# Kernel tuning notes

Measured on AMD Instinct MI355X. Metric: run time of the kernel, lower is better.

Reference implementation:

```python
import jax, jax.numpy as jnp
import numpy as np
from jax import lax

B_SZ, L, D, N, R = 1, 4096, 768, 16, 48  # R = dt_rank = ceil(D/16)


def _soft_clamp(x, lo=1e-4, hi=10.0):
    center = (hi + lo) / 2.0
    half_range = (hi - lo) / 2.0
    return center + half_range * jnp.tanh((x - center) / half_range)


def setup_inputs() -> dict:
    key = jax.random.key(0)
    ks = jax.random.split(key, 6)
    x = jax.random.normal(ks[0], (B_SZ, L, D), jnp.float32)
    # A_log init: log(1..N) broadcast over D (HiPPO-style S4D-real init)
    A_log = jnp.log(jnp.broadcast_to(jnp.arange(1, N + 1, dtype=jnp.float32), (D, N)))
    D_param = jnp.ones((D,), jnp.float32)
    # lecun_normal kernels
    W_bc = jax.random.normal(ks[1], (D, 2 * N), jnp.float32) / np.sqrt(D).astype(np.float32)
    W_dt = jax.random.normal(ks[2], (D, R), jnp.float32) / np.sqrt(D).astype(np.float32)
    W_dtp = jax.random.normal(ks[3], (R, D), jnp.float32) / np.sqrt(R).astype(np.float32)
    # dt bias init: inverse-softplus of uniform(dt_min, dt_max)
    dt = jax.random.uniform(ks[4], (D,), jnp.float32, 0.001, 0.1)
    dt = jnp.clip(dt, 1e-4)
    b_dt = dt + jnp.log(-jnp.expm1(-dt))
    rms_scale = jnp.ones((D,), jnp.float32)  # RMSNorm learnable scale
    return {"x": x, "A_log": A_log, "D_param": D_param, "W_bc": W_bc,
            "W_dt": W_dt, "W_dtp": W_dtp, "b_dt": b_dt, "rms_scale": rms_scale}


def reference(x, A_log, D_param, W_bc, W_dt, W_dtp, b_dt, rms_scale):
    n = A_log.shape[1]
    A = -jnp.exp(A_log)                                   # (D, N)
    bc = x @ W_bc                                         # (B, L, 2N)
    B_sel, C_sel = bc[..., :n], bc[..., n:]               # (B, L, N) each
    # delta = softplus(dt_proj(x_dt)) -> RMSNorm -> soft_clamp  (tustin mode)
    delta = jax.nn.softplus((x @ W_dt) @ W_dtp + b_dt)    # (B, L, D)
    delta = delta * lax.rsqrt(jnp.mean(delta * delta, axis=-1, keepdims=True) + 1e-6) * rms_scale
    delta = _soft_clamp(delta, 1e-4, 10.0)
    # Bilinear (Tustin) discretization, all fp32 already
    dE = delta[..., None]                                 # (B, L, D, 1)
    half = 0.5 * dE * A                                   # (B, L, D, N)
    denom = 1.0 - half
    A_bar = (1.0 + half) / denom                          # (B, L, D, N)
    B_bar = jnp.sqrt(dE) * B_sel[:, :, None, :] / denom   # (B, L, D, N)
    # trapezoidal input averaging
    x_prev = jnp.concatenate([jnp.zeros_like(x[:, :1]), x[:, :-1]], axis=1)
    x_in = 0.5 * (x + x_prev)                             # (B, L, D)
    Bx = B_bar * x_in[..., None]                          # (B, L, D, N)

    def op(left, right):
        a_l, b_l = left
        a_r, b_r = right
        return (a_r * a_l, a_r * b_l + b_r)

    _, all_h = lax.associative_scan(op, (A_bar, Bx), axis=1)
    y = jnp.sum(C_sel[:, :, None, :] * all_h, axis=-1)    # (B, L, D)
    return y + D_param * x
```

## Files before the change

### kernel.cpp

```cpp
#include <hip/hip_runtime.h>
#include <math.h>

#define LSEQ 4096
#define DD 768
#define NST 16
#define RNK 48
#define TCH 64
#define NCH (LSEQ / TCH)
#define KSTEPS 24
#define NTILES 5
#define WFRAG_N (KSTEPS * NTILES * 64 * 8)
#define WDTP_N  (2 * RNK * 64 * 8)

typedef __attribute__((ext_vector_type(8))) short bf16x8;
typedef __attribute__((ext_vector_type(4))) float f32x4;

__device__ __forceinline__ float softplus_f(float z) {
    float e = __expf(-fabsf(z));
    return fmaxf(z, 0.0f) + __logf(1.0f + e);
}

__device__ __forceinline__ float tanh_fast(float w) {
    float t = __expf(2.0f * fabsf(w));
    float r = 1.0f - 2.0f / (t + 1.0f);
    return copysignf(r, w);
}

__device__ __forceinline__ float soft_clamp_f(float v) {
    const float ctr = 5.00005f;
    const float hr  = 4.99995f;
    const float inv_hr = 1.0f / 4.99995f;
    return ctr + hr * tanh_fast((v - ctr) * inv_hr);
}

__device__ __forceinline__ float wave_sum(float v) {
    #pragma unroll
    for (int m = 32; m >= 1; m >>= 1) v += __shfl_xor(v, m, 64);
    return v;
}

__device__ __forceinline__ unsigned short rne_bf16(float v) {
    unsigned u = __float_as_uint(v);
    return (unsigned short)((u + 0x7FFFu + ((u >> 16) & 1u)) >> 16);
}

__global__ __launch_bounds__(256) void k_prep(
    const float* __restrict__ W_dt, const float* __restrict__ W_bc,
    const float* __restrict__ W_dtp,
    unsigned short* __restrict__ wf_hi, unsigned short* __restrict__ wf_lo,
    unsigned short* __restrict__ wp_hi, unsigned short* __restrict__ wp_lo)
{
    int i = blockIdx.x * 256 + threadIdx.x;
    if (i < WFRAG_N) {
        int j  = i & 7;
        int l  = (i >> 3) & 63;
        int nk = i >> 9;
        int n  = nk % NTILES;
        int kk = nk / NTILES;
        int k   = kk * 32 + (l >> 4) * 8 + j;
        int col = n * 16 + (l & 15);
        float v = (col < RNK) ? W_dt[k * RNK + col] : W_bc[k * 32 + (col - RNK)];
        unsigned short h = rne_bf16(v);
        float hf = __uint_as_float((unsigned)h << 16);
        wf_hi[i] = h;
        wf_lo[i] = rne_bf16(v - hf);
    } else if (i < WFRAG_N + WDTP_N) {
        int ii = i - WFRAG_N;
        int j  = ii & 7;
        int l  = (ii >> 3) & 63;
        int nk = ii >> 9;
        int n  = nk % RNK;
        int ks = nk / RNK;
        int k   = ks * 32 + (l >> 4) * 8 + j;
        int col = n * 16 + (l & 15);
        float v = (k < RNK) ? W_dtp[k * DD + col] : 0.f;
        unsigned short h = rne_bf16(v);
        float hf = __uint_as_float((unsigned)h << 16);
        wp_hi[ii] = h;
        wp_lo[ii] = rne_bf16(v - hf);
    }
}

__global__ __launch_bounds__(512) void k_proj_mfma(
    const float* __restrict__ x,
    const unsigned short* __restrict__ wf_hi,
    const unsigned short* __restrict__ wf_lo,
    const unsigned short* __restrict__ wp_hi,
    const unsigned short* __restrict__ wp_lo,
    const float* __restrict__ b_dt, const float* __restrict__ rms_scale,
    float* __restrict__ sq_out, float* __restrict__ bc_out)
{
    __shared__ __align__(16) float smem[16 * 772];
    __shared__ __align__(16) float t_lds[16][RNK];
    __shared__ float red2[8][16];

    const int tid  = threadIdx.x;
    const int lane = tid & 63;
    const int wq   = tid >> 6;
    const int mt   = blockIdx.x;

    {
        const float4* xg = (const float4*)(x + (size_t)mt * 16 * DD);
        #pragma unroll 2
        for (int idx = tid; idx < 3072; idx += 512) {
            int r = idx / 192, c4 = idx - r * 192;
            *(float4*)&smem[r * 772 + c4 * 4] = xg[idx];
        }
    }
    __syncthreads();

    const int rloc = lane & 15;
    const int ko   = (lane >> 4) * 8;

    f32x4 acc[NTILES];
    #pragma unroll
    for (int n = 0; n < NTILES; ++n) acc[n] = (f32x4){0.f, 0.f, 0.f, 0.f};

    #pragma unroll
    for (int k3 = 0; k3 < 3; ++k3) {
        const int kk = wq * 3 + k3;
        const float* xp = &smem[rloc * 772 + kk * 32 + ko];
        float4 xa = *(const float4*)xp;
        float4 xb = *(const float4*)(xp + 4);
        float va[8] = {xa.x, xa.y, xa.z, xa.w, xb.x, xb.y, xb.z, xb.w};
        bf16x8 ah, al;
        #pragma unroll
        for (int j = 0; j < 8; ++j) {
            unsigned short h = rne_bf16(va[j]);
            float hf = __uint_as_float((unsigned)h << 16);
            ah[j] = (short)h;
            al[j] = (short)rne_bf16(va[j] - hf);
        }
        const int base = kk * (NTILES * 512) + lane * 8;
        #pragma unroll
        for (int n = 0; n < NTILES; ++n) {
            bf16x8 bh = *(const bf16x8*)(wf_hi + base + n * 512);
            bf16x8 bl = *(const bf16x8*)(wf_lo + base + n * 512);
            acc[n] = __builtin_amdgcn_mfma_f32_16x16x32_bf16(al, bh, acc[n], 0, 0, 0);
            acc[n] = __builtin_amdgcn_mfma_f32_16x16x32_bf16(ah, bl, acc[n], 0, 0, 0);
            acc[n] = __builtin_amdgcn_mfma_f32_16x16x32_bf16(ah, bh, acc[n], 0, 0, 0);
        }
    }
    __syncthreads();

    if (wq > 0) {
        float* red = smem + ((wq - 1) * 64 + lane) * 20;
        #pragma unroll
        for (int n = 0; n < NTILES; ++n)
            #pragma unroll
            for (int r = 0; r < 4; ++r) red[n * 4 + r] = acc[n][r];
    }
    __syncthreads();
    if (wq == 0) {
        #pragma unroll
        for (int w = 0; w < 7; ++w) {
            const float* red = smem + (w * 64 + lane) * 20;
            #pragma unroll
            for (int n = 0; n < NTILES; ++n)
                #pragma unroll
                for (int r = 0; r < 4; ++r) acc[n][r] += red[n * 4 + r];
        }
        const int r0 = (lane >> 4) * 4;
        const int cb = lane & 15;
        #pragma unroll
        for (int n = 0; n < 3; ++n)
            #pragma unroll
            for (int r = 0; r < 4; ++r)
                t_lds[r0 + r][n * 16 + cb] = acc[n][r];
        #pragma unroll
        for (int n = 3; n < 5; ++n)
            #pragma unroll
            for (int r = 0; r < 4; ++r)
                bc_out[(size_t)(mt * 16 + r0 + r) * 32 + (n - 3) * 16 + cb] = acc[n][r];
    }
    __syncthreads();

    bf16x8 tah[2], tal[2];
    #pragma unroll
    for (int ks = 0; ks < 2; ++ks) {
        const int kbase = ks * 32 + ko;
        float tv[8];
        #pragma unroll
        for (int j = 0; j < 8; ++j)
            tv[j] = (kbase + j < RNK) ? t_lds[rloc][kbase + j] : 0.f;
        #pragma unroll
        for (int j = 0; j < 8; ++j) {
            unsigned short h = rne_bf16(tv[j]);
            float hf = __uint_as_float((unsigned)h << 16);
            tah[ks][j] = (short)h;
            tal[ks][j] = (short)rne_bf16(tv[j] - hf);
        }
    }

    const int r0 = (lane >> 4) * 4;
    #pragma unroll
    for (int nn = 0; nn < 6; ++nn) {
        const int n = wq * 6 + nn;
        f32x4 z = (f32x4){0.f, 0.f, 0.f, 0.f};
        {
            const int b0 = n * 512 + lane * 8;
            bf16x8 bh = *(const bf16x8*)(wp_hi + b0);
            bf16x8 bl = *(const bf16x8*)(wp_lo + b0);
            z = __builtin_amdgcn_mfma_f32_16x16x32_bf16(tal[0], bh, z, 0, 0, 0);
            z = __builtin_amdgcn_mfma_f32_16x16x32_bf16(tah[0], bl, z, 0, 0, 0);
            z = __builtin_amdgcn_mfma_f32_16x16x32_bf16(tah[0], bh, z, 0, 0, 0);
        }
        {
            const int b1 = (RNK + n) * 512 + lane * 8;
            bf16x8 bh = *(const bf16x8*)(wp_hi + b1);
            bf16x8 bl = *(const bf16x8*)(wp_lo + b1);
            z = __builtin_amdgcn_mfma_f32_16x16x32_bf16(tal[1], bh, z, 0, 0, 0);
            z = __builtin_amdgcn_mfma_f32_16x16x32_bf16(tah[1], bl, z, 0, 0, 0);
            z = __builtin_amdgcn_mfma_f32_16x16x32_bf16(tah[1], bh, z, 0, 0, 0);
        }
        const int col = n * 16 + (lane & 15);
        const float bb = b_dt[col];
        #pragma unroll
        for (int r = 0; r < 4; ++r)
            smem[(r0 + r) * 772 + col] = softplus_f(z[r] + bb);
    }
    __syncthreads();

    const int d0 = tid;
    const int d1 = tid + 512;
    const bool has2 = (tid < 256);
    {
        float sp0[16], sp1[16];
        #pragma unroll
        for (int li = 0; li < 16; ++li) {
            sp0[li] = smem[li * 772 + d0];
            sp1[li] = has2 ? smem[li * 772 + d1] : 0.f;
        }
        #pragma unroll
        for (int li = 0; li < 16; ++li) {
            float ss = wave_sum(sp0[li] * sp0[li] + sp1[li] * sp1[li]);
            if (lane == 0) red2[wq][li] = ss;
        }
        __syncthreads();
        float rs0 = rms_scale[d0];
        float rs1 = has2 ? rms_scale[d1] : 0.f;
        #pragma unroll
        for (int li = 0; li < 16; ++li) {
            float tot = 0.f;
            #pragma unroll
            for (int k = 0; k < 8; ++k) tot += red2[k][li];
            float inv = rsqrtf(tot * (1.0f / DD) + 1e-6f);
            size_t rowoff = (size_t)(mt * 16 + li) * DD;
            sq_out[rowoff + d0] = sqrtf(soft_clamp_f(sp0[li] * inv * rs0));
            if (has2)
                sq_out[rowoff + d1] = sqrtf(soft_clamp_f(sp1[li] * inv * rs1));
        }
    }
}

__global__ __launch_bounds__(256, 4) void k_scan1(
    const float* __restrict__ x, const float* __restrict__ sqd,
    const float* __restrict__ bc, const float* __restrict__ A_log,
    float* __restrict__ Pbuf, float* __restrict__ Hbuf)
{
    __shared__ __align__(16) float xs[(TCH + 1) * 64];
    __shared__ __align__(16) float sqv[TCH * 64];
    __shared__ __align__(16) float bs[TCH * 16];

    const int tid = threadIdx.x;
    const int db  = blockIdx.x * 64;
    const int c   = blockIdx.y;
    const int l0  = c * TCH;

    for (int i = tid; i < (TCH + 1) * 16; i += 256) {
        int r = i >> 4, f = i & 15;
        int l = l0 - 1 + r;
        float4 v = (l >= 0) ? *(const float4*)&x[(size_t)l * DD + db + f * 4]
                            : make_float4(0.f, 0.f, 0.f, 0.f);
        *(float4*)&xs[r * 64 + f * 4] = v;
    }
    for (int i = tid; i < TCH * 16; i += 256) {
        int r = i >> 4, f = i & 15;
        *(float4*)&sqv[r * 64 + f * 4] =
            *(const float4*)&sqd[(size_t)(l0 + r) * DD + db + f * 4];
    }
    for (int i = tid; i < TCH * 4; i += 256) {
        int r = i >> 2, f = i & 3;
        *(float4*)&bs[r * 16 + f * 4] =
            *(const float4*)&bc[(size_t)(l0 + r) * 32 + f * 4];
    }

    const int lane = tid & 63;
    const int w    = tid >> 6;
    const int q    = lane >> 4;
    const int dlo  = (lane & 15) + w * 16;
    const int d    = db + dlo;

    float An[4];
    {
        float4 a = *(const float4*)&A_log[d * NST + q * 4];
        An[0] = -__expf(a.x); An[1] = -__expf(a.y);
        An[2] = -__expf(a.z); An[3] = -__expf(a.w);
    }
    __syncthreads();

    float h[4]  = {0.f, 0.f, 0.f, 0.f};
    float Pp[4] = {1.f, 1.f, 1.f, 1.f};
    float xprev = xs[dlo];

    #pragma unroll 4
    for (int ll = 0; ll < TCH; ++ll) {
        float xv = xs[(ll + 1) * 64 + dlo];
        float sq = sqv[ll * 64 + dlo];
        float4 Bc = *(const float4*)&bs[ll * 16 + q * 4];

        float xin = 0.5f * (xv + xprev);
        xprev = xv;
        float c0 = 0.5f * sq * sq;
        float c1 = sq * xin;

        float dn0 = fmaf(-c0, An[0], 1.0f);
        float dn1 = fmaf(-c0, An[1], 1.0f);
        float dn2 = fmaf(-c0, An[2], 1.0f);
        float dn3 = fmaf(-c0, An[3], 1.0f);
        float m01 = dn0 * dn1, m23 = dn2 * dn3;
        float ip  = __builtin_amdgcn_rcpf(m01 * m23);
        float ip01 = ip * m23, ip23 = ip * m01;
        float iv0 = ip01 * dn1, iv1 = ip01 * dn0;
        float iv2 = ip23 * dn3, iv3 = ip23 * dn2;
        float t10 = 2.0f - dn0, t11 = 2.0f - dn1;
        float t12 = 2.0f - dn2, t13 = 2.0f - dn3;

        Pp[0] *= t10 * iv0;
        Pp[1] *= t11 * iv1;
        Pp[2] *= t12 * iv2;
        Pp[3] *= t13 * iv3;
        h[0] = fmaf(t10, h[0], c1 * Bc.x) * iv0;
        h[1] = fmaf(t11, h[1], c1 * Bc.y) * iv1;
        h[2] = fmaf(t12, h[2], c1 * Bc.z) * iv2;
        h[3] = fmaf(t13, h[3], c1 * Bc.w) * iv3;
    }
    #pragma unroll
    for (int n = 0; n < 4; ++n) {
        int idx = (c * NST + q * 4 + n) * DD + d;
        Pbuf[idx] = Pp[n];
        Hbuf[idx] = h[n];
    }
}

__global__ __launch_bounds__(64) void k_scan2(
    float* __restrict__ Pbuf, const float* __restrict__ Hbuf)
{
    const int s = blockIdx.x * 64 + threadIdx.x;
    const int d = s % DD;
    const int n = s / DD;
    const int stride = NST * DD;

    int idx = n * DD + d;
    int idx_pf = idx;
    float p[8], h[8];
    #pragma unroll
    for (int i = 0; i < 8; ++i) {
        p[i] = Pbuf[idx_pf];
        h[i] = Hbuf[idx_pf];
        idx_pf += stride;
    }

    float carry = 0.f;
    for (int g = 0; g < NCH / 8; ++g) {
        float pn[8], hn[8];
        if (g + 1 < NCH / 8) {
            #pragma unroll
            for (int i = 0; i < 8; ++i) {
                pn[i] = Pbuf[idx_pf];
                hn[i] = Hbuf[idx_pf];
                idx_pf += stride;
            }
        }
        #pragma unroll
        for (int i = 0; i < 8; ++i) {
            Pbuf[idx] = carry;
            carry = fmaf(p[i], carry, h[i]);
            idx += stride;
        }
        #pragma unroll
        for (int i = 0; i < 8; ++i) { p[i] = pn[i]; h[i] = hn[i]; }
    }
}

__global__ __launch_bounds__(256, 4) void k_scan3(
    const float* __restrict__ x, const float* __restrict__ sqd,
    const float* __restrict__ bc, const float* __restrict__ A_log,
    const float* __restrict__ carryin, const float* __restrict__ D_param,
    float* __restrict__ out)
{
    __shared__ __align__(16) float xs[(TCH + 1) * 64];
    __shared__ __align__(16) float sqv[TCH * 64];
    __shared__ __align__(16) float bs[TCH * 32];

    const int tid = threadIdx.x;
    const int db  = blockIdx.x * 64;
    const int c   = blockIdx.y;
    const int l0  = c * TCH;

    for (int i = tid; i < (TCH + 1) * 16; i += 256) {
        int r = i >> 4, f = i & 15;
        int l = l0 - 1 + r;
        float4 v = (l >= 0) ? *(const float4*)&x[(size_t)l * DD + db + f * 4]
                            : make_float4(0.f, 0.f, 0.f, 0.f);
        *(float4*)&xs[r * 64 + f * 4] = v;
    }
    for (int i = tid; i < TCH * 16; i += 256) {
        int r = i >> 4, f = i & 15;
        *(float4*)&sqv[r * 64 + f * 4] =
            *(const float4*)&sqd[(size_t)(l0 + r) * DD + db + f * 4];
    }
    for (int i = tid; i < TCH * 8; i += 256) {
        int r = i >> 3, f = i & 7;
        *(float4*)&bs[r * 32 + f * 4] =
            *(const float4*)&bc[(size_t)(l0 + r) * 32 + f * 4];
    }

    const int lane = tid & 63;
    const int w    = tid >> 6;
    const int q    = lane >> 4;
    const int dlo  = (lane & 15) + w * 16;
    const int d    = db + dlo;

    float An[4];
    {
        float4 a = *(const float4*)&A_log[d * NST + q * 4];
        An[0] = -__expf(a.x); An[1] = -__expf(a.y);
        An[2] = -__expf(a.z); An[3] = -__expf(a.w);
    }
    float h[4];
    #pragma unroll
    for (int n = 0; n < 4; ++n)
        h[n] = carryin[(c * NST + q * 4 + n) * DD + d];
    const float Dp = D_param[d];

    __syncthreads();

    float xprev = xs[dlo];
    #pragma unroll 4
    for (int ll = 0; ll < TCH; ++ll) {
        float xv = xs[(ll + 1) * 64 + dlo];
        float sq = sqv[ll * 64 + dlo];
        float4 Bc = *(const float4*)&bs[ll * 32 + q * 4];
        float4 Cc = *(const float4*)&bs[ll * 32 + 16 + q * 4];

        float xin = 0.5f * (xv + xprev);
        xprev = xv;
        float c0 = 0.5f * sq * sq;
        float c1 = sq * xin;

        float dn0 = fmaf(-c0, An[0], 1.0f);
        float dn1 = fmaf(-c0, An[1], 1.0f);
        float dn2 = fmaf(-c0, An[2], 1.0f);
        float dn3 = fmaf(-c0, An[3], 1.0f);
        float m01 = dn0 * dn1, m23 = dn2 * dn3;
        float ip  = __builtin_amdgcn_rcpf(m01 * m23);
        float ip01 = ip * m23, ip23 = ip * m01;
        float iv0 = ip01 * dn1, iv1 = ip01 * dn0;
        float iv2 = ip23 * dn3, iv3 = ip23 * dn2;
        float t10 = 2.0f - dn0, t11 = 2.0f - dn1;
        float t12 = 2.0f - dn2, t13 = 2.0f - dn3;

        h[0] = fmaf(t10, h[0], c1 * Bc.x) * iv0;
        h[1] = fmaf(t11, h[1], c1 * Bc.y) * iv1;
        h[2] = fmaf(t12, h[2], c1 * Bc.z) * iv2;
        h[3] = fmaf(t13, h[3], c1 * Bc.w) * iv3;

        float y = h[0] * Cc.x;
        y = fmaf(h[1], Cc.y, y);
        y = fmaf(h[2], Cc.z, y);
        y = fmaf(h[3], Cc.w, y);

        y += __shfl_xor(y, 16, 64);
        y += __shfl_xor(y, 32, 64);
        if (q == 0)
            out[(size_t)(l0 + ll) * DD + d] = fmaf(Dp, xv, y);
    }
}

extern "C" void kernel_launch(void* const* d_in, const int* in_sizes, int n_in,
                              void* d_out, int out_size, void* d_ws, size_t ws_size,
                              hipStream_t stream) {
    const float* x         = (const float*)d_in[0];
    const float* A_log     = (const float*)d_in[1];
    const float* D_param   = (const float*)d_in[2];
    const float* W_bc      = (const float*)d_in[3];
    const float* W_dt      = (const float*)d_in[4];
    const float* W_dtp     = (const float*)d_in[5];
    const float* b_dt      = (const float*)d_in[6];
    const float* rms_scale = (const float*)d_in[7];
    float* out = (float*)d_out;

    float* ws    = (float*)d_ws;
    float* sqbuf = ws;
    float* bcbuf = sqbuf + (size_t)LSEQ * DD;
    float* Pbuf  = bcbuf + (size_t)LSEQ * 32;
    float* Hbuf  = Pbuf + (size_t)NCH * NST * DD;
    unsigned short* wf_hi = (unsigned short*)(Hbuf + (size_t)NCH * NST * DD);
    unsigned short* wf_lo = wf_hi + WFRAG_N;
    unsigned short* wp_hi = wf_lo + WFRAG_N;
    unsigned short* wp_lo = wp_hi + WDTP_N;

    k_prep<<<(WFRAG_N + WDTP_N + 255) / 256, 256, 0, stream>>>(
        W_dt, W_bc, W_dtp, wf_hi, wf_lo, wp_hi, wp_lo);
    k_proj_mfma<<<LSEQ / 16, 512, 0, stream>>>(x, wf_hi, wf_lo, wp_hi, wp_lo,
                                               b_dt, rms_scale, sqbuf, bcbuf);
    k_scan1<<<dim3(DD / 64, NCH), 256, 0, stream>>>(x, sqbuf, bcbuf, A_log,
                                                    Pbuf, Hbuf);
    k_scan2<<<(DD * NST) / 64, 64, 0, stream>>>(Pbuf, Hbuf);
    k_scan3<<<dim3(DD / 64, NCH), 256, 0, stream>>>(x, sqbuf, bcbuf, A_log,
                                                    Pbuf, D_param, out);
}
```

Before: 75.02 us.

## Precompute per-step scan coefficients in projection kernel instead of x/sqrt-delta

The projection kernel now writes the two per-step coefficients c0 = delta/2 and c1 = sqrt(delta)*trapezoidal x input, computed from an x tile it keeps in shared memory. Both scan kernels load these instead of recomputing them from x and sqrt(delta), which removes the x staging from scan1. Scan3 reads x directly from global memory per step for the D skip term. In exchange the workspace holds an extra L×D buffer, so the projection kernel writes and both scans read more bytes, and the projection kernel's shared memory doubles, which may reduce its occupancy.

```diff
diff --git a/kernel.cpp b/kernel.cpp
--- a/kernel.cpp
+++ b/kernel.cpp
@@ -88,9 +88,11 @@
     const unsigned short* __restrict__ wp_hi,
     const unsigned short* __restrict__ wp_lo,
     const float* __restrict__ b_dt, const float* __restrict__ rms_scale,
-    float* __restrict__ sq_out, float* __restrict__ bc_out)
+    float* __restrict__ c0_out, float* __restrict__ c1_out,
+    float* __restrict__ bc_out)
 {
-    __shared__ __align__(16) float smem[16 * 772];
+    __shared__ __align__(16) float smem_x[16 * 772];
+    __shared__ __align__(16) float smem_sp[16 * 772];
     __shared__ __align__(16) float t_lds[16][RNK];
     __shared__ float red2[8][16];
 
@@ -104,7 +106,7 @@
         #pragma unroll 2
         for (int idx = tid; idx < 3072; idx += 512) {
             int r = idx / 192, c4 = idx - r * 192;
-            *(float4*)&smem[r * 772 + c4 * 4] = xg[idx];
+            *(float4*)&smem_x[r * 772 + c4 * 4] = xg[idx];
         }
     }
     __syncthreads();
@@ -119,7 +121,7 @@
     #pragma unroll
     for (int k3 = 0; k3 < 3; ++k3) {
         const int kk = wq * 3 + k3;
-        const float* xp = &smem[rloc * 772 + kk * 32 + ko];
+        const float* xp = &smem_x[rloc * 772 + kk * 32 + ko];
         float4 xa = *(const float4*)xp;
         float4 xb = *(const float4*)(xp + 4);
         float va[8] = {xa.x, xa.y, xa.z, xa.w, xb.x, xb.y, xb.z, xb.w};
@@ -144,7 +146,7 @@
     __syncthreads();
 
     if (wq > 0) {
-        float* red = smem + ((wq - 1) * 64 + lane) * 20;
+        float* red = smem_sp + ((wq - 1) * 64 + lane) * 20;
         #pragma unroll
         for (int n = 0; n < NTILES; ++n)
             #pragma unroll
@@ -154,7 +156,7 @@
     if (wq == 0) {
         #pragma unroll
         for (int w = 0; w < 7; ++w) {
-            const float* red = smem + (w * 64 + lane) * 20;
+            const float* red = smem_sp + (w * 64 + lane) * 20;
             #pragma unroll
             for (int n = 0; n < NTILES; ++n)
                 #pragma unroll
@@ -217,7 +219,7 @@
         const float bb = b_dt[col];
         #pragma unroll
         for (int r = 0; r < 4; ++r)
-            smem[(r0 + r) * 772 + col] = softplus_f(z[r] + bb);
+            smem_sp[(r0 + r) * 772 + col] = softplus_f(z[r] + bb);
     }
     __syncthreads();
 
@@ -228,8 +230,8 @@
         float sp0[16], sp1[16];
         #pragma unroll
         for (int li = 0; li < 16; ++li) {
-            sp0[li] = smem[li * 772 + d0];
-            sp1[li] = has2 ? smem[li * 772 + d1] : 0.f;
+            sp0[li] = smem_sp[li * 772 + d0];
+            sp1[li] = has2 ? smem_sp[li * 772 + d1] : 0.f;
         }
         #pragma unroll
         for (int li = 0; li < 16; ++li) {
@@ -239,6 +241,8 @@
         __syncthreads();
         float rs0 = rms_scale[d0];
         float rs1 = has2 ? rms_scale[d1] : 0.f;
+        float xm0 = (mt > 0) ? x[(size_t)(mt * 16 - 1) * DD + d0] : 0.f;
+        float xm1 = (has2 && mt > 0) ? x[(size_t)(mt * 16 - 1) * DD + d1] : 0.f;
         #pragma unroll
         for (int li = 0; li < 16; ++li) {
             float tot = 0.f;
@@ -246,20 +250,31 @@
             for (int k = 0; k < 8; ++k) tot += red2[k][li];
             float inv = rsqrtf(tot * (1.0f / DD) + 1e-6f);
             size_t rowoff = (size_t)(mt * 16 + li) * DD;
-            sq_out[rowoff + d0] = sqrtf(soft_clamp_f(sp0[li] * inv * rs0));
-            if (has2)
-                sq_out[rowoff + d1] = sqrtf(soft_clamp_f(sp1[li] * inv * rs1));
+
+            float dl0 = soft_clamp_f(sp0[li] * inv * rs0);
+            float xl0 = smem_x[li * 772 + d0];
+            float xp0 = (li == 0) ? xm0 : smem_x[(li - 1) * 772 + d0];
+            c0_out[rowoff + d0] = 0.5f * dl0;
+            c1_out[rowoff + d0] = sqrtf(dl0) * 0.5f * (xl0 + xp0);
+
+            if (has2) {
+                float dl1 = soft_clamp_f(sp1[li] * inv * rs1);
+                float xl1 = smem_x[li * 772 + d1];
+                float xp1 = (li == 0) ? xm1 : smem_x[(li - 1) * 772 + d1];
+                c0_out[rowoff + d1] = 0.5f * dl1;
+                c1_out[rowoff + d1] = sqrtf(dl1) * 0.5f * (xl1 + xp1);
+            }
         }
     }
 }
 
 __global__ __launch_bounds__(256, 4) void k_scan1(
-    const float* __restrict__ x, const float* __restrict__ sqd,
+    const float* __restrict__ c0b, const float* __restrict__ c1b,
     const float* __restrict__ bc, const float* __restrict__ A_log,
     float* __restrict__ Pbuf, float* __restrict__ Hbuf)
 {
-    __shared__ __align__(16) float xs[(TCH + 1) * 64];
-    __shared__ __align__(16) float sqv[TCH * 64];
+    __shared__ __align__(16) float c0v[TCH * 64];
+    __shared__ __align__(16) float c1v[TCH * 64];
     __shared__ __align__(16) float bs[TCH * 16];
 
     const int tid = threadIdx.x;
@@ -267,17 +282,12 @@
     const int c   = blockIdx.y;
     const int l0  = c * TCH;
 
-    for (int i = tid; i < (TCH + 1) * 16; i += 256) {
-        int r = i >> 4, f = i & 15;
-        int l = l0 - 1 + r;
-        float4 v = (l >= 0) ? *(const float4*)&x[(size_t)l * DD + db + f * 4]
-                            : make_float4(0.f, 0.f, 0.f, 0.f);
-        *(float4*)&xs[r * 64 + f * 4] = v;
-    }
     for (int i = tid; i < TCH * 16; i += 256) {
         int r = i >> 4, f = i & 15;
-        *(float4*)&sqv[r * 64 + f * 4] =
-            *(const float4*)&sqd[(size_t)(l0 + r) * DD + db + f * 4];
+        *(float4*)&c0v[r * 64 + f * 4] =
+            *(const float4*)&c0b[(size_t)(l0 + r) * DD + db + f * 4];
+        *(float4*)&c1v[r * 64 + f * 4] =
+            *(const float4*)&c1b[(size_t)(l0 + r) * DD + db + f * 4];
     }
     for (int i = tid; i < TCH * 4; i += 256) {
         int r = i >> 2, f = i & 3;
@@ -301,18 +311,12 @@
 
     float h[4]  = {0.f, 0.f, 0.f, 0.f};
     float Pp[4] = {1.f, 1.f, 1.f, 1.f};
-    float xprev = xs[dlo];
 
     #pragma unroll 4
     for (int ll = 0; ll < TCH; ++ll) {
-        float xv = xs[(ll + 1) * 64 + dlo];
-        float sq = sqv[ll * 64 + dlo];
+        float c0 = c0v[ll * 64 + dlo];
+        float c1 = c1v[ll * 64 + dlo];
         float4 Bc = *(const float4*)&bs[ll * 16 + q * 4];
-
-        float xin = 0.5f * (xv + xprev);
-        xprev = xv;
-        float c0 = 0.5f * sq * sq;
-        float c1 = sq * xin;
 
         float dn0 = fmaf(-c0, An[0], 1.0f);
         float dn1 = fmaf(-c0, An[1], 1.0f);
@@ -384,13 +388,13 @@
 }
 
 __global__ __launch_bounds__(256, 4) void k_scan3(
-    const float* __restrict__ x, const float* __restrict__ sqd,
-    const float* __restrict__ bc, const float* __restrict__ A_log,
-    const float* __restrict__ carryin, const float* __restrict__ D_param,
-    float* __restrict__ out)
+    const float* __restrict__ x, const float* __restrict__ c0b,
+    const float* __restrict__ c1b, const float* __restrict__ bc,
+    const float* __restrict__ A_log, const float* __restrict__ carryin,
+    const float* __restrict__ D_param, float* __restrict__ out)
 {
-    __shared__ __align__(16) float xs[(TCH + 1) * 64];
-    __shared__ __align__(16) float sqv[TCH * 64];
+    __shared__ __align__(16) float c0v[TCH * 64];
+    __shared__ __align__(16) float c1v[TCH * 64];
     __shared__ __align__(16) float bs[TCH * 32];
 
     const int tid = threadIdx.x;
@@ -398,17 +402,12 @@
     const int c   = blockIdx.y;
     const int l0  = c * TCH;
 
-    for (int i = tid; i < (TCH + 1) * 16; i += 256) {
-        int r = i >> 4, f = i & 15;
-        int l = l0 - 1 + r;
-        float4 v = (l >= 0) ? *(const float4*)&x[(size_t)l * DD + db + f * 4]
-                            : make_float4(0.f, 0.f, 0.f, 0.f);
-        *(float4*)&xs[r * 64 + f * 4] = v;
-    }
     for (int i = tid; i < TCH * 16; i += 256) {
         int r = i >> 4, f = i & 15;
-        *(float4*)&sqv[r * 64 + f * 4] =
-            *(const float4*)&sqd[(size_t)(l0 + r) * DD + db + f * 4];
+        *(float4*)&c0v[r * 64 + f * 4] =
+            *(const float4*)&c0b[(size_t)(l0 + r) * DD + db + f * 4];
+        *(float4*)&c1v[r * 64 + f * 4] =
+            *(const float4*)&c1b[(size_t)(l0 + r) * DD + db + f * 4];
     }
     for (int i = tid; i < TCH * 8; i += 256) {
         int r = i >> 3, f = i & 7;
@@ -436,18 +435,17 @@
 
     __syncthreads();
 
-    float xprev = xs[dlo];
+    float xv_n = x[(size_t)l0 * DD + d];
     #pragma unroll 4
     for (int ll = 0; ll < TCH; ++ll) {
-        float xv = xs[(ll + 1) * 64 + dlo];
-        float sq = sqv[ll * 64 + dlo];
+        float xv = xv_n;
+        const int lnx = (l0 + ll + 1 < LSEQ) ? l0 + ll + 1 : l0 + ll;
+        xv_n = x[(size_t)lnx * DD + d];
+
+        float c0 = c0v[ll * 64 + dlo];
+        float c1 = c1v[ll * 64 + dlo];
         float4 Bc = *(const float4*)&bs[ll * 32 + q * 4];
         float4 Cc = *(const float4*)&bs[ll * 32 + 16 + q * 4];
-
-        float xin = 0.5f * (xv + xprev);
-        xprev = xv;
-        float c0 = 0.5f * sq * sq;
-        float c1 = sq * xin;
 
         float dn0 = fmaf(-c0, An[0], 1.0f);
         float dn1 = fmaf(-c0, An[1], 1.0f);
@@ -492,8 +490,9 @@
     float* out = (float*)d_out;
 
     float* ws    = (float*)d_ws;
-    float* sqbuf = ws;
-    float* bcbuf = sqbuf + (size_t)LSEQ * DD;
+    float* c0buf = ws;
+    float* c1buf = c0buf + (size_t)LSEQ * DD;
+    float* bcbuf = c1buf + (size_t)LSEQ * DD;
     float* Pbuf  = bcbuf + (size_t)LSEQ * 32;
     float* Hbuf  = Pbuf + (size_t)NCH * NST * DD;
     unsigned short* wf_hi = (unsigned short*)(Hbuf + (size_t)NCH * NST * DD);
@@ -504,10 +503,11 @@
     k_prep<<<(WFRAG_N + WDTP_N + 255) / 256, 256, 0, stream>>>(
         W_dt, W_bc, W_dtp, wf_hi, wf_lo, wp_hi, wp_lo);
     k_proj_mfma<<<LSEQ / 16, 512, 0, stream>>>(x, wf_hi, wf_lo, wp_hi, wp_lo,
-                                               b_dt, rms_scale, sqbuf, bcbuf);
-    k_scan1<<<dim3(DD / 64, NCH), 256, 0, stream>>>(x, sqbuf, bcbuf, A_log,
+                                               b_dt, rms_scale, c0buf, c1buf,
+                                               bcbuf);
+    k_scan1<<<dim3(DD / 64, NCH), 256, 0, stream>>>(c0buf, c1buf, bcbuf, A_log,
                                                     Pbuf, Hbuf);
     k_scan2<<<(DD * NST) / 64, 64, 0, stream>>>(Pbuf, Hbuf);
-    k_scan3<<<dim3(DD / 64, NCH), 256, 0, stream>>>(x, sqbuf, bcbuf, A_log,
-                                                    Pbuf, D_param, out);
-}
+    k_scan3<<<dim3(DD / 64, NCH), 256, 0, stream>>>(x, c0buf, c1buf, bcbuf,
+                                                    A_log, Pbuf, D_param, out);
+}
```

Result: no change. 74.62 us (-0.5%).
